# Optimization experiments

Measured on AMD Instinct MI355X. Metric: run time of the kernel, lower is better.

## Reference

```python
import jax, jax.numpy as jnp
import numpy as np

B, C, H, W = 8, 2, 256, 256


def edt2d(mask):
    """Exact Euclidean distance transform, scipy.ndimage.distance_transform_edt semantics:
    for nonzero (True) pixels, distance to the nearest zero pixel. mask: bool [B,H,W]."""
    b, h, w = mask.shape
    INF = jnp.float32(1e4)  # larger than any achievable in-image distance
    m = jnp.moveaxis(mask, 1, 0)  # [H,B,W]

    def step(carry, mm):
        d = jnp.where(mm, carry + 1.0, 0.0)
        return d, d

    init = jnp.full((b, w), INF, jnp.float32)
    _, fwd = jax.lax.scan(step, init, m)            # top-down 1D column distance
    _, bwd = jax.lax.scan(step, init, m[::-1])      # bottom-up
    g = jnp.minimum(fwd, bwd[::-1])                 # [H,B,W] vertical nearest-zero distance
    g2 = jnp.moveaxis(g, 0, 1) ** 2                 # [B,H,W]

    j = jnp.arange(w, dtype=jnp.float32)
    D2 = (j[:, None] - j[None, :]) ** 2             # [W,W] horizontal squared offsets

    def per_image(gi):                              # gi: [H,W] squared column distances
        # d[i,j] = sqrt(min_k g2[i,k] + (j-k)^2)  -- exact separable EDT
        return jnp.sqrt(jnp.min(gi[:, None, :] + D2[None, :, :], axis=-1))

    return jax.lax.map(per_image, g2)               # sequence over batch to bound memory


def setup_inputs() -> dict:
    key = jax.random.key(0)
    k1, k2 = jax.random.split(key)
    preds = jax.random.normal(k1, (B, C, H, W), dtype=jnp.float32)
    target = jax.random.randint(k2, (B, H, W), 0, 2, dtype=jnp.int32)
    return {"preds": preds, "target": target}


def reference(preds, target):
    # ignore_index handling: replace 255 with target.min() (no-op when 255 absent)
    tmin = target.min()
    target = jnp.where(target == 255, tmin, target)
    gt = target.astype(jnp.float32)

    # softmax then argmax over class dim (== argmax of logits)
    pc = jnp.argmax(jax.nn.softmax(preds, axis=1), axis=1).astype(jnp.float32)  # [B,H,W]

    # EDT(pos) + EDT(neg), done under no_grad in the original
    pc_dist = jax.lax.stop_gradient(edt2d(pc > 0) + edt2d(pc == 0))
    gt_dist = jax.lax.stop_gradient(edt2d(gt > 0) + edt2d(gt == 0))

    pred_error = jnp.abs(gt - pc)                   # sqrt((gt-pc)^2)
    dist = jnp.sqrt(pc_dist ** 2 + gt_dist ** 2)
    multipled = jnp.sqrt(pred_error * dist + 1e-9)
    return multipled.mean()
```

## Files before the change

kernel.cpp:

```cpp
#include <hip/hip_runtime.h>
#include <cfloat>

#define BB 8
#define CC 2
#define HH 256
#define WW 256

typedef unsigned long long ull;

static constexpr float EDT_INF = 1e4f;
static constexpr int   NPIX    = BB * HH * WW;

__device__ __forceinline__ float g2_of(const ull* m, int pos, bool set) {
    if (!set) return 0.0f;
    float fwd = EDT_INF + (float)(pos + 1);
    {
        int k = pos - 1;
        if (k >= 0) {
            int w = k >> 6;
            ull t = ~m[w] & (~0ULL >> (63 - (k & 63)));
            for (;;) {
                if (t) { int j = (w << 6) + 63 - __builtin_clzll(t); fwd = (float)(pos - j); break; }
                if (--w < 0) break;
                t = ~m[w];
            }
        }
    }
    float bwd = EDT_INF + (float)(256 - pos);
    {
        int k = pos + 1;
        if (k < 256) {
            int w = k >> 6;
            ull t = ~m[w] & (~0ULL << (k & 63));
            for (;;) {
                if (t) { int j = (w << 6) + __builtin_ctzll(t); bwd = (float)(j - pos); break; }
                if (++w >= 4) break;
                t = ~m[w];
            }
        }
    }
    float g = fminf(fwd, bwd);
    return g * g;
}

__global__ void k_masks(const float* __restrict__ preds,
                        const int*   __restrict__ target,
                        ull* __restrict__ mPC, ull* __restrict__ mGT0,
                        ull* __restrict__ mG255, int* __restrict__ tminPart) {
    const int blk = blockIdx.x;
    const int b  = blk >> 5;
    const int ig = blk & 31;
    const int wv = threadIdx.x >> 6;
    const int ln = threadIdx.x & 63;
    const int w  = (wv << 6) | ln;

    int tmin = 0x7fffffff;
#pragma unroll
    for (int r = 0; r < 8; ++r) {
        int i = ig * 8 + r;
        float a0 = preds[((size_t)b * CC + 0) * HH * WW + (size_t)i * WW + w];
        float a1 = preds[((size_t)b * CC + 1) * HH * WW + (size_t)i * WW + w];
        bool pc = (a1 > a0);
        int tv = target[((size_t)b * HH + i) * WW + w];
        tmin = min(tmin, tv);
        ull bp = __ballot(pc);
        ull b0 = __ballot(tv > 0);
        ull b2 = __ballot(tv == 255);
        if (ln == 0) {
            size_t midx = ((size_t)b * HH + i) * 4 + wv;
            mPC[midx] = bp; mGT0[midx] = b0; mG255[midx] = b2;
        }
    }
    for (int off = 32; off > 0; off >>= 1) tmin = min(tmin, __shfl_down(tmin, off));
    __shared__ int swv[4];
    if (ln == 0) swv[wv] = tmin;
    __syncthreads();
    if (threadIdx.x == 0)
        tminPart[blk] = min(min(swv[0], swv[1]), min(swv[2], swv[3]));
}

__global__ void k_fused(const int* __restrict__ target,
                        const ull* __restrict__ mPC,
                        const ull* __restrict__ mGT0,
                        const ull* __restrict__ mG255,
                        const int* __restrict__ tminPart,
                        float* __restrict__ partials) {
    const int blk = blockIdx.x;
    const int b = blk >> 8, j = blk & 255;
    const int i = threadIdx.x;
    const int wv = i >> 6, ln = i & 63;

    __shared__ int stw[4];
    {
        int v = tminPart[i];
        for (int off = 32; off > 0; off >>= 1) v = min(v, __shfl_down(v, off));
        if (ln == 0) stw[wv] = v;
    }
    __syncthreads();
    const int tmin = min(min(stw[0], stw[1]), min(stw[2], stw[3]));
    const bool allpos = (tmin > 0);

    ull wp[4], wg[4], np[4], ng[4];
    {
        const ull* pP = mPC   + ((size_t)b * HH + i) * 4;
        const ull* p0 = mGT0  + ((size_t)b * HH + i) * 4;
        const ull* p2 = mG255 + ((size_t)b * HH + i) * 4;
#pragma unroll
        for (int k = 0; k < 4; ++k) {
            wp[k] = pP[k];
            ull g = p0[k];
            if (!allpos) g &= ~p2[k];
            wg[k] = g;
            np[k] = ~wp[k]; ng[k] = ~wg[k];
        }
    }
    bool pc = (wp[j >> 6] >> (j & 63)) & 1ULL;
    bool gt = (wg[j >> 6] >> (j & 63)) & 1ULL;

    __shared__ float s_pm[HH], s_pn[HH], s_gm[HH], s_gn[HH];
    s_pm[i] = g2_of(wp, j, pc);
    s_pn[i] = g2_of(np, j, !pc);
    s_gm[i] = g2_of(wg, j, gt);
    s_gn[i] = g2_of(ng, j, !gt);
    __syncthreads();

    const float* rv = pc ? s_pm : s_pn;
    const float* rw = gt ? s_gm : s_gn;
    float mn = rv[i];
    float mg = rw[i];
    for (int d = 1; d < HH; ++d) {
        float dd = (float)(d * d);
        if (__all((dd >= mn) & (dd >= mg))) break;
        int kl = i - d, kr = i + d;
        if (kl >= 0) { mn = fminf(mn, dd + rv[kl]); mg = fminf(mg, dd + rw[kl]); }
        if (kr < HH) { mn = fminf(mn, dd + rv[kr]); mg = fminf(mg, dd + rw[kr]); }
    }
    float pd = sqrtf(mn);
    float gd = sqrtf(mg);

    int tv = target[((size_t)b * HH + i) * WW + j];
    if (tv == 255) tv = tmin;
    float gtv = (float)tv;
    float pcv = pc ? 1.0f : 0.0f;
    float err  = fabsf(gtv - pcv);
    float dist = sqrtf(pd * pd + gd * gd);
    float mult = sqrtf(err * dist + 1e-9f);

    __shared__ float sws[4];
    for (int off = 32; off > 0; off >>= 1) mult += __shfl_down(mult, off);
    if (ln == 0) sws[wv] = mult;
    __syncthreads();
    if (i == 0) partials[blk] = ((sws[0] + sws[1]) + sws[2]) + sws[3];
}

__global__ void k_final(const float* __restrict__ partials, float* __restrict__ out) {
    __shared__ float s[256];
    float acc = 0.0f;
    for (int k = threadIdx.x; k < BB * WW; k += 256) acc += partials[k];
    s[threadIdx.x] = acc;
    __syncthreads();
    for (int st = 128; st > 0; st >>= 1) {
        if (threadIdx.x < st) s[threadIdx.x] += s[threadIdx.x + st];
        __syncthreads();
    }
    if (threadIdx.x == 0) out[0] = s[0] * (1.0f / (float)NPIX);
}

extern "C" void kernel_launch(void* const* d_in, const int* in_sizes, int n_in,
                              void* d_out, int out_size, void* d_ws, size_t ws_size,
                              hipStream_t stream) {
    const float* preds  = (const float*)d_in[0];
    const int*   target = (const int*)d_in[1];
    float* out = (float*)d_out;

    ull* mPC   = (ull*)d_ws;
    ull* mGT0  = mPC  + (size_t)BB * HH * 4;
    ull* mG255 = mGT0 + (size_t)BB * HH * 4;
    float* partials = (float*)(mG255 + (size_t)BB * HH * 4);
    int*   tminPart = (int*)(partials + BB * WW);

    k_masks<<<256, 256, 0, stream>>>(preds, target, mPC, mGT0, mG255, tminPart);
    k_fused<<<BB * WW, HH, 0, stream>>>(target, mPC, mGT0, mG255, tminPart, partials);
    k_final<<<1, 256, 0, stream>>>(partials, out);
}
```

Measured before the change: 25.14 us.

## Bound per-pixel EDT column scan by nearest opposite pixel in column

Result: no change. 25.46 us (+1.3%).

```diff
diff --git a/kernel.cpp b/kernel.cpp
--- a/kernel.cpp
+++ b/kernel.cpp
@@ -11,18 +11,17 @@
 static constexpr float EDT_INF = 1e4f;
 static constexpr int   NPIX    = BB * HH * WW;
 
-__device__ __forceinline__ float g2_of(const ull* m, int pos, bool set) {
-    if (!set) return 0.0f;
+__device__ __forceinline__ float hdist2(const ull* zm, int pos) {
     float fwd = EDT_INF + (float)(pos + 1);
     {
         int k = pos - 1;
         if (k >= 0) {
             int w = k >> 6;
-            ull t = ~m[w] & (~0ULL >> (63 - (k & 63)));
+            ull t = zm[w] & (~0ULL >> (63 - (k & 63)));
             for (;;) {
                 if (t) { int j = (w << 6) + 63 - __builtin_clzll(t); fwd = (float)(pos - j); break; }
                 if (--w < 0) break;
-                t = ~m[w];
+                t = zm[w];
             }
         }
     }
@@ -31,16 +30,45 @@
         int k = pos + 1;
         if (k < 256) {
             int w = k >> 6;
-            ull t = ~m[w] & (~0ULL << (k & 63));
+            ull t = zm[w] & (~0ULL << (k & 63));
             for (;;) {
                 if (t) { int j = (w << 6) + __builtin_ctzll(t); bwd = (float)(j - pos); break; }
                 if (++w >= 4) break;
-                t = ~m[w];
+                t = zm[w];
             }
         }
     }
     float g = fminf(fwd, bwd);
     return g * g;
+}
+
+__device__ __forceinline__ int nearest_set(const ull* zm, int pos) {
+    int best = 1 << 20;
+    {
+        int k = pos - 1;
+        if (k >= 0) {
+            int w = k >> 6;
+            ull t = zm[w] & (~0ULL >> (63 - (k & 63)));
+            for (;;) {
+                if (t) { int j = (w << 6) + 63 - __builtin_clzll(t); best = pos - j; break; }
+                if (--w < 0) break;
+                t = zm[w];
+            }
+        }
+    }
+    {
+        int k = pos + 1;
+        if (k < 256) {
+            int w = k >> 6;
+            ull t = zm[w] & (~0ULL << (k & 63));
+            for (;;) {
+                if (t) { int j = (w << 6) + __builtin_ctzll(t); best = min(best, j - pos); break; }
+                if (++w >= 4) break;
+                t = zm[w];
+            }
+        }
+    }
+    return best;
 }
 
 __global__ void k_masks(const float* __restrict__ preds,
@@ -100,7 +128,7 @@
     const int tmin = min(min(stw[0], stw[1]), min(stw[2], stw[3]));
     const bool allpos = (tmin > 0);
 
-    ull wp[4], wg[4], np[4], ng[4];
+    ull wp[4], wg[4];
     {
         const ull* pP = mPC   + ((size_t)b * HH + i) * 4;
         const ull* p0 = mGT0  + ((size_t)b * HH + i) * 4;
@@ -111,31 +139,67 @@
             ull g = p0[k];
             if (!allpos) g &= ~p2[k];
             wg[k] = g;
-            np[k] = ~wp[k]; ng[k] = ~wg[k];
-        }
-    }
-    bool pc = (wp[j >> 6] >> (j & 63)) & 1ULL;
-    bool gt = (wg[j >> 6] >> (j & 63)) & 1ULL;
-
-    __shared__ float s_pm[HH], s_pn[HH], s_gm[HH], s_gn[HH];
-    s_pm[i] = g2_of(wp, j, pc);
-    s_pn[i] = g2_of(np, j, !pc);
-    s_gm[i] = g2_of(wg, j, gt);
-    s_gn[i] = g2_of(ng, j, !gt);
-    __syncthreads();
-
-    const float* rv = pc ? s_pm : s_pn;
-    const float* rw = gt ? s_gm : s_gn;
-    float mn = rv[i];
-    float mg = rw[i];
-    for (int d = 1; d < HH; ++d) {
-        float dd = (float)(d * d);
-        if (__all((dd >= mn) & (dd >= mg))) break;
-        int kl = i - d, kr = i + d;
-        if (kl >= 0) { mn = fminf(mn, dd + rv[kl]); mg = fminf(mg, dd + rw[kl]); }
-        if (kr < HH) { mn = fminf(mn, dd + rv[kr]); mg = fminf(mg, dd + rw[kr]); }
+        }
+    }
+    const bool pc = (wp[j >> 6] >> (j & 63)) & 1ULL;
+    const bool gt = (wg[j >> 6] >> (j & 63)) & 1ULL;
+
+    ull zp[4], zg[4];
+#pragma unroll
+    for (int k = 0; k < 4; ++k) {
+        zp[k] = pc ? ~wp[k] : wp[k];
+        zg[k] = gt ? ~wg[k] : wg[k];
+    }
+
+    __shared__ float s_p[HH], s_g[HH];
+    __shared__ ull cshP[4], cshG[4];
+    s_p[i] = hdist2(zp, j);
+    s_g[i] = hdist2(zg, j);
+    {
+        ull bp = __ballot(pc);
+        ull bg = __ballot(gt);
+        if (ln == 0) { cshP[wv] = bp; cshG[wv] = bg; }
+    }
+    __syncthreads();
+
+    ull cp[4], cg[4];
+#pragma unroll
+    for (int k = 0; k < 4; ++k) {
+        ull P = cshP[k], G = cshG[k];
+        cp[k] = pc ? ~P : P;
+        cg[k] = gt ? ~G : G;
+    }
+    const int dvp = nearest_set(cp, i);
+    const int dvg = nearest_set(cg, i);
+
+    float mn = s_p[i];
+    {
+        int dmax = min(dvp, HH);
+        for (int d = 1; d < dmax; ++d) {
+            float dd = (float)(d * d);
+            if (dd >= mn) break;
+            int kl = i - d, kr = i + d;
+            if (kl >= 0) mn = fminf(mn, dd + s_p[kl]);
+            if (kr < HH) mn = fminf(mn, dd + s_p[kr]);
+        }
+        float dv = (float)dvp;
+        mn = fminf(mn, dv * dv);
     }
     float pd = sqrtf(mn);
+
+    float mg = s_g[i];
+    {
+        int dmax = min(dvg, HH);
+        for (int d = 1; d < dmax; ++d) {
+            float dd = (float)(d * d);
+            if (dd >= mg) break;
+            int kl = i - d, kr = i + d;
+            if (kl >= 0) mg = fminf(mg, dd + s_g[kl]);
+            if (kr < HH) mg = fminf(mg, dd + s_g[kr]);
+        }
+        float dv = (float)dvg;
+        mg = fminf(mg, dv * dv);
+    }
     float gd = sqrtf(mg);
 
     int tv = target[((size_t)b * HH + i) * WW + j];
```
